# Kernel tuning notes

Hardware: AMD Instinct MI355X
Metric: run time of the kernel (lower is better)

The kernel has to match this reference:

```python
import jax, jax.numpy as jnp
import numpy as np

N_NODES = 50000
N_EDGES = 800000
N_GRAPHS = 256
F_IN = 256
H_DIM = 64


def setup_inputs() -> dict:
    key = jax.random.key(0)
    ks = jax.random.split(key, 9)
    x = jax.random.normal(ks[0], (N_NODES, F_IN), dtype=jnp.float32)
    edge_index = jax.random.randint(ks[1], (2, N_EDGES), 0, N_NODES, dtype=jnp.int64)
    batch = jnp.sort(jax.random.randint(ks[2], (N_NODES,), 0, N_GRAPHS, dtype=jnp.int64))
    s = 1.0 / np.sqrt(F_IN)
    Wq = jax.random.normal(ks[3], (F_IN, H_DIM), dtype=jnp.float32) * s
    bq = jnp.zeros((H_DIM,), dtype=jnp.float32)
    Wk = jax.random.normal(ks[4], (F_IN, H_DIM), dtype=jnp.float32) * s
    bk = jnp.zeros((H_DIM,), dtype=jnp.float32)
    Wv = jax.random.normal(ks[5], (F_IN, H_DIM), dtype=jnp.float32) * s
    bv = jnp.zeros((H_DIM,), dtype=jnp.float32)
    return {"x": x, "Wq": Wq, "bq": bq, "Wk": Wk, "bk": bk, "Wv": Wv, "bv": bv,
            "edge_index": edge_index, "batch": batch}


def reference(x, Wq, bq, Wk, bk, Wv, bv, edge_index, batch):
    src, dest = edge_index[0], edge_index[1]
    # node projections then per-edge gathers
    q = (x @ Wq + bq)[dest]            # [E, h]
    k = (x @ Wk + bk)[src]             # [E, h]
    v = (x @ Wv + bv)[src]             # [E, h]
    # per-edge dot-product score (bmm of [E,1,h] x [E,h,1])
    prod = jnp.sum(k * q, axis=-1, keepdims=True) / np.sqrt(H_DIM)  # [E, 1]
    exp = jnp.exp(prod)
    seg = batch[src]                   # per-graph segment of source node
    denom = jax.ops.segment_sum(exp, seg, num_segments=N_GRAPHS)    # [G, 1]
    a = exp / (denom[seg] + 1e-6)      # [E, 1]
    out = jax.ops.segment_sum(v * a, dest, num_segments=N_NODES)    # [N, h]
    return out
```

## Files before the change

### kernel.cpp

```cpp
#include <hip/hip_runtime.h>

#define H    64
#define F    256
#define NSEG 256
#define SCB  2048
#define MB   64
#define KC   64
#define XPAD 72

typedef float          f32x4v __attribute__((ext_vector_type(4)));
typedef short          bf16x8 __attribute__((ext_vector_type(8)));
typedef unsigned short u16x4  __attribute__((ext_vector_type(4)));

__global__ __launch_bounds__(256) void hist_kernel(
    const int* __restrict__ ei, int* __restrict__ counts8, int N, int E)
{
    const int pbase = (blockIdx.x & 7) * N;
    const int e0 = blockIdx.x * 1024 + threadIdx.x * 4;
    if (e0 + 3 < E) {
        const int4 d4 = *(const int4*)(ei + E + e0);
        atomicAdd(&counts8[pbase + min(max(d4.x, 0), N - 1)], 1);
        atomicAdd(&counts8[pbase + min(max(d4.y, 0), N - 1)], 1);
        atomicAdd(&counts8[pbase + min(max(d4.z, 0), N - 1)], 1);
        atomicAdd(&counts8[pbase + min(max(d4.w, 0), N - 1)], 1);
    } else {
        for (int e = e0; e < E; ++e) {
            int dst = ei[E + e];
            atomicAdd(&counts8[pbase + min(max(dst, 0), N - 1)], 1);
        }
    }
}

#define CVT_WRITE(buf, rr, cc, val) do {                                      \
    const float ff_[4] = {(val).x, (val).y, (val).z, (val).w};                \
    u16x4 h_, l_;                                                             \
    _Pragma("unroll")                                                         \
    for (int u_ = 0; u_ < 4; ++u_) {                                          \
        unsigned ub_ = __float_as_uint(ff_[u_]);                              \
        h_[u_] = (unsigned short)(ub_ >> 16);                                 \
        float rf_ = ff_[u_] - __uint_as_float(ub_ & 0xFFFF0000u);             \
        l_[u_] = (unsigned short)(__float_as_uint(rf_) >> 16);                \
    }                                                                         \
    *(u16x4*)&xs_hi[buf][(rr) * XPAD + (cc) * 4] = h_;                        \
    *(u16x4*)&xs_lo[buf][(rr) * XPAD + (cc) * 4] = l_;                        \
} while (0)

__global__ __launch_bounds__(768, 3) void qkv_mfma(
    const float* __restrict__ x,
    const float* __restrict__ Wq, const float* __restrict__ Wk,
    const float* __restrict__ Wv,
    const float* __restrict__ bq, const float* __restrict__ bk,
    const float* __restrict__ bv,
    float* __restrict__ q, float* __restrict__ k, float* __restrict__ v,
    int N, int ntiles)
{
    __shared__ unsigned short xs_hi[2][MB * XPAD];
    __shared__ unsigned short xs_lo[2][MB * XPAD];

    const int t    = threadIdx.x;
    const int lane = t & 63;
    const int w    = t >> 6;
    const int mat  = w >> 2;
    const int ct   = w & 3;
    const int l15  = lane & 15;
    const int quad = lane >> 4;

    const float* Wm   = (mat == 0) ? Wq : (mat == 1) ? Wk : Wv;
    const float* bias = (mat == 0) ? bq : (mat == 1) ? bk : bv;
    float*       dst  = (mat == 0) ? q  : (mat == 1) ? k  : v;
    const int col = ct * 16 + l15;
    const float bb = bias[col];

    bf16x8 Bh[8], Bl[8];
    #pragma unroll
    for (int u = 0; u < 8; ++u) {
        #pragma unroll
        for (int j = 0; j < 8; ++j) {
            const float f = Wm[(size_t)(u * 32 + quad * 8 + j) * H + col];
            const unsigned ub = __float_as_uint(f);
            Bh[u][j] = (short)(ub >> 16);
            const float rf = f - __uint_as_float(ub & 0xFFFF0000u);
            Bl[u][j] = (short)(__float_as_uint(rf) >> 16);
        }
    }

    const int r0 = t >> 4;
    const int c0 = t & 15;
    const int r1 = (t + 768) >> 4;

    #pragma unroll 1
    for (int tile = blockIdx.x; tile < ntiles; tile += gridDim.x) {
        const int block0 = tile * MB;

        f32x4v acc[4];
        #pragma unroll
        for (int i = 0; i < 4; ++i) acc[i] = (f32x4v)0.f;

        float4 pv0, pv1;
        pv0 = *(const float4*)(x + (size_t)min(block0 + r0, N - 1) * F + c0 * 4);
        if (t < 256)
            pv1 = *(const float4*)(x + (size_t)min(block0 + r1, N - 1) * F + c0 * 4);
        CVT_WRITE(0, r0, c0, pv0);
        if (t < 256) CVT_WRITE(0, r1, c0, pv1);

        #pragma unroll
        for (int c = 0; c < 4; ++c) {
            __syncthreads();

            if (c < 3) {
                const int kb = (c + 1) * KC;
                pv0 = *(const float4*)(x + (size_t)min(block0 + r0, N - 1) * F + kb + c0 * 4);
                if (t < 256)
                    pv1 = *(const float4*)(x + (size_t)min(block0 + r1, N - 1) * F + kb + c0 * 4);
            }

            #pragma unroll
            for (int sk = 0; sk < 2; ++sk) {
                const int u = c * 2 + sk;
                #pragma unroll
                for (int mt = 0; mt < 4; ++mt) {
                    const int ao = (mt * 16 + l15) * XPAD + sk * 32 + quad * 8;
                    const bf16x8 ah = *(const bf16x8*)&xs_hi[c & 1][ao];
                    const bf16x8 al = *(const bf16x8*)&xs_lo[c & 1][ao];
                    f32x4v a = acc[mt];
                    a = __builtin_amdgcn_mfma_f32_16x16x32_bf16(ah, Bh[u], a, 0, 0, 0);
                    a = __builtin_amdgcn_mfma_f32_16x16x32_bf16(ah, Bl[u], a, 0, 0, 0);
                    a = __builtin_amdgcn_mfma_f32_16x16x32_bf16(al, Bh[u], a, 0, 0, 0);
                    acc[mt] = a;
                }
            }

            if (c < 3) {
                const int nb = (c & 1) ^ 1;
                CVT_WRITE(nb, r0, c0, pv0);
                if (t < 256) CVT_WRITE(nb, r1, c0, pv1);
            }
        }

        #pragma unroll
        for (int mt = 0; mt < 4; ++mt) {
            #pragma unroll
            for (int r = 0; r < 4; ++r) {
                const int node = block0 + mt * 16 + quad * 4 + r;
                if (node < N)
                    dst[(size_t)node * H + col] = acc[mt][r] + bb;
            }
        }
    }
}

__global__ __launch_bounds__(256) void scanA(
    const int* __restrict__ counts8, int* __restrict__ counts,
    int* __restrict__ offsets, int* __restrict__ bsum, int n)
{
    __shared__ int ps[256];
    const int t = threadIdx.x;
    const int i0 = blockIdx.x * SCB + t * 8;
    int loc[8];
    int s = 0;
    #pragma unroll
    for (int u = 0; u < 8; ++u) {
        int i = i0 + u;
        int c = 0;
        if (i < n) {
            #pragma unroll
            for (int p = 0; p < 8; ++p) c += counts8[p * n + i];
            counts[i] = c;
            c = (c + 3) & ~3;
        }
        loc[u] = s; s += c;
    }
    ps[t] = s;
    __syncthreads();
    for (int off = 1; off < 256; off <<= 1) {
        int a = (t >= off) ? ps[t - off] : 0;
        __syncthreads();
        ps[t] += a;
        __syncthreads();
    }
    const int base = ps[t] - s;
    #pragma unroll
    for (int u = 0; u < 8; ++u) {
        int i = i0 + u;
        if (i < n) offsets[i] = base + loc[u];
    }
    if (t == 255) bsum[blockIdx.x] = ps[255];
}

__global__ void scanB(int* __restrict__ bsum, int nb)
{
    const int t = threadIdx.x;
    int v = (t < nb) ? bsum[t] : 0;
    int inc = v;
    #pragma unroll
    for (int off = 1; off < 64; off <<= 1) {
        int u = __shfl_up(inc, off, 64);
        if (t >= off) inc += u;
    }
    if (t < nb) bsum[t] = inc - v;
}

__global__ __launch_bounds__(256) void scanC(
    const int* __restrict__ bsum, const int* __restrict__ counts8,
    int* __restrict__ offsets, int* __restrict__ cursor8, int n)
{
    const int i0 = blockIdx.x * SCB + threadIdx.x * 8;
    const int add = bsum[blockIdx.x];
    #pragma unroll
    for (int u = 0; u < 8; ++u) {
        int i = i0 + u;
        if (i < n) {
            int o = offsets[i] + add;
            offsets[i] = o;
            #pragma unroll
            for (int p = 0; p < 8; ++p) {
                cursor8[p * n + i] = o;
                o += counts8[p * n + i];
            }
        }
    }
}

__global__ __launch_bounds__(256) void reorder_kernel(
    const int* __restrict__ ei, const int* __restrict__ batch,
    int* __restrict__ cursor8, unsigned* __restrict__ epack, int E, int N)
{
    const int pbase = (blockIdx.x & 7) * N;
    int e = blockIdx.x * 1024 + threadIdx.x;
    #pragma unroll
    for (int u = 0; u < 4; ++u) {
        if (e < E) {
            int src = ei[e];
            int dst = ei[E + e];
            src = min(max(src, 0), N - 1);
            dst = min(max(dst, 0), N - 1);
            int seg = batch[src];
            seg = min(max(seg, 0), NSEG - 1);
            int pos = atomicAdd(&cursor8[pbase + dst], 1);
            epack[pos] = (unsigned)src | ((unsigned)seg << 16);
        }
        e += 256;
    }
}

__global__ __launch_bounds__(256) void score_kernel(
    const float* __restrict__ q, const float* __restrict__ k,
    const unsigned* __restrict__ epack,
    const int* __restrict__ offsets, const int* __restrict__ counts,
    float* __restrict__ exps, float* __restrict__ denom8, int N)
{
    __shared__ float sden[NSEG];
    const int t = threadIdx.x;
    sden[t] = 0.f;
    __syncthreads();

    const int lane16 = t & 15;
    const int grp    = (t >> 4) & 3;
    const int wave   = t >> 6;
    const int nwaves = gridDim.x * 4;

    const float4* q4 = (const float4*)q;
    const float4* k4 = (const float4*)k;

    for (int n = blockIdx.x * 4 + wave; n < N; n += nwaves) {
        const int off = offsets[n];
        const int cnt = counts[n];
        if (cnt == 0) continue;
        const float4 qv = q4[(size_t)n * 16 + lane16];
        for (int i = grp; i < cnt; i += 4) {
            const int pos = off + i;
            const unsigned p = epack[pos];
            const int src = p & 0xFFFF;
            const float4 kv = k4[(size_t)src * 16 + lane16];
            float d = kv.x * qv.x + kv.y * qv.y + kv.z * qv.z + kv.w * qv.w;
            d += __shfl_xor(d, 1, 64);
            d += __shfl_xor(d, 2, 64);
            d += __shfl_xor(d, 4, 64);
            d += __shfl_xor(d, 8, 64);
            if (lane16 == 0) {
                float ex = __expf(d * 0.125f);
                exps[pos] = ex;
                atomicAdd(&sden[(p >> 16) & 255], ex);
            }
        }
    }
    __syncthreads();
    float ds = sden[t];
    if (ds != 0.f) atomicAdd(&denom8[(blockIdx.x & 7) * NSEG + t], ds);
}

__global__ __launch_bounds__(256) void accum_kernel(
    const float* __restrict__ v, const float* __restrict__ exps,
    const unsigned* __restrict__ epack,
    const int* __restrict__ offsets, const int* __restrict__ counts,
    const float* __restrict__ denom8, float* __restrict__ out, int N)
{
    __shared__ float rden[NSEG];
    const int t = threadIdx.x;
    {
        float dsum = 0.f;
        #pragma unroll
        for (int p = 0; p < 8; ++p) dsum += denom8[p * NSEG + t];
        rden[t] = 1.0f / (dsum + 1e-6f);
    }
    __syncthreads();

    const int lane = t & 63;
    const int wave = t >> 6;
    const int n = blockIdx.x * 4 + wave;
    if (n >= N) return;

    const int off = offsets[n];
    const int cnt = counts[n];

    float acc = 0.f;
    int i = 0;
    for (; i + 8 <= cnt; i += 8) {
        const uint4  pa = *(const uint4*)(epack + off + i);
        const uint4  pb = *(const uint4*)(epack + off + i + 4);
        const float4 ea = *(const float4*)(exps + off + i);
        const float4 eb = *(const float4*)(exps + off + i + 4);
        const float v0 = v[(size_t)(pa.x & 0xFFFF) * H + lane];
        const float v1 = v[(size_t)(pa.y & 0xFFFF) * H + lane];
        const float v2 = v[(size_t)(pa.z & 0xFFFF) * H + lane];
        const float v3 = v[(size_t)(pa.w & 0xFFFF) * H + lane];
        const float v4_ = v[(size_t)(pb.x & 0xFFFF) * H + lane];
        const float v5 = v[(size_t)(pb.y & 0xFFFF) * H + lane];
        const float v6 = v[(size_t)(pb.z & 0xFFFF) * H + lane];
        const float v7 = v[(size_t)(pb.w & 0xFFFF) * H + lane];
        acc = fmaf(v0, ea.x * rden[(pa.x >> 16) & 255], acc);
        acc = fmaf(v1, ea.y * rden[(pa.y >> 16) & 255], acc);
        acc = fmaf(v2, ea.z * rden[(pa.z >> 16) & 255], acc);
        acc = fmaf(v3, ea.w * rden[(pa.w >> 16) & 255], acc);
        acc = fmaf(v4_, eb.x * rden[(pb.x >> 16) & 255], acc);
        acc = fmaf(v5, eb.y * rden[(pb.y >> 16) & 255], acc);
        acc = fmaf(v6, eb.z * rden[(pb.z >> 16) & 255], acc);
        acc = fmaf(v7, eb.w * rden[(pb.w >> 16) & 255], acc);
    }
    for (; i + 4 <= cnt; i += 4) {
        const uint4  pp = *(const uint4*)(epack + off + i);
        const float4 ee = *(const float4*)(exps + off + i);
        const float v0 = v[(size_t)(pp.x & 0xFFFF) * H + lane];
        const float v1 = v[(size_t)(pp.y & 0xFFFF) * H + lane];
        const float v2 = v[(size_t)(pp.z & 0xFFFF) * H + lane];
        const float v3 = v[(size_t)(pp.w & 0xFFFF) * H + lane];
        acc = fmaf(v0, ee.x * rden[(pp.x >> 16) & 255], acc);
        acc = fmaf(v1, ee.y * rden[(pp.y >> 16) & 255], acc);
        acc = fmaf(v2, ee.z * rden[(pp.z >> 16) & 255], acc);
        acc = fmaf(v3, ee.w * rden[(pp.w >> 16) & 255], acc);
    }
    for (; i < cnt; ++i) {
        const unsigned p = epack[off + i];
        acc = fmaf(v[(size_t)(p & 0xFFFF) * H + lane],
                   exps[off + i] * rden[(p >> 16) & 255], acc);
    }
    out[(size_t)n * H + lane] = acc;
}

extern "C" void kernel_launch(void* const* d_in, const int* in_sizes, int n_in,
                              void* d_out, int out_size, void* d_ws, size_t ws_size,
                              hipStream_t stream)
{
    const float* x   = (const float*)d_in[0];
    const float* Wq  = (const float*)d_in[1];
    const float* bq  = (const float*)d_in[2];
    const float* Wk  = (const float*)d_in[3];
    const float* bk  = (const float*)d_in[4];
    const float* Wv  = (const float*)d_in[5];
    const float* bv  = (const float*)d_in[6];
    const int* ei    = (const int*)d_in[7];
    const int* batch = (const int*)d_in[8];

    const int N = in_sizes[8];
    const int E = in_sizes[7] / 2;
    const int EP = E + 3 * N + 16;

    float*    q       = (float*)d_ws;
    float*    k       = q + (size_t)N * H;
    float*    v       = k + (size_t)N * H;
    float*    exps    = v + (size_t)N * H;
    unsigned* epack   = (unsigned*)(exps + EP);
    int*      counts  = (int*)(epack + EP);
    int*      offsets = counts + N;
    int*      bsum    = offsets + N;
    float*    denom8  = (float*)(bsum + 64);

    int* counts8 = (int*)epack;
    int* cursor8 = (int*)exps;

    hipMemsetAsync(counts8, 0, 8 * (size_t)N * sizeof(int), stream);
    hipMemsetAsync(denom8, 0, 8 * NSEG * sizeof(float), stream);

    const int NT = (N + MB - 1) / MB;
    const int EB = (E + 1023) / 1024;
    const int NBSC = (N + SCB - 1) / SCB;

    hist_kernel<<<EB, 256, 0, stream>>>(ei, counts8, N, E);

    qkv_mfma<<<256, 768, 0, stream>>>(
        x, Wq, Wk, Wv, bq, bk, bv, q, k, v, N, NT);

    scanA<<<NBSC, 256, 0, stream>>>(counts8, counts, offsets, bsum, N);
    scanB<<<1, 64, 0, stream>>>(bsum, NBSC);
    scanC<<<NBSC, 256, 0, stream>>>(bsum, counts8, offsets, cursor8, N);

    reorder_kernel<<<(E + 1023) / 1024, 256, 0, stream>>>(
        ei, batch, cursor8, epack, E, N);

    score_kernel<<<2048, 256, 0, stream>>>(
        q, k, epack, offsets, counts, exps, denom8, N);

    accum_kernel<<<(N + 3) / 4, 256, 0, stream>>>(
        v, exps, epack, offsets, counts, denom8, (float*)d_out, N);
}
```

Baseline: 298.9 us.

## Replace 8-way privatized histogram with destination-range partitioned single counters

The hist and reorder kernels no longer keep eight private copies of the per-node counters and cursors. Each edge chunk is now processed by eight blocks, and each block only handles destinations inside its own node span, so there is a single counts and cursor array. This shrinks the memset and the scan work (no 8-way reductions or cursor expansions) and keeps atomics within a narrower address range, which should help cache locality. In exchange, the destination indices are read eight times and there are eight times as many blocks.

```diff
diff --git a/kernel.cpp b/kernel.cpp
--- a/kernel.cpp
+++ b/kernel.cpp
@@ -13,20 +13,25 @@
 typedef unsigned short u16x4  __attribute__((ext_vector_type(4)));
 
 __global__ __launch_bounds__(256) void hist_kernel(
-    const int* __restrict__ ei, int* __restrict__ counts8, int N, int E)
-{
-    const int pbase = (blockIdx.x & 7) * N;
-    const int e0 = blockIdx.x * 1024 + threadIdx.x * 4;
+    const int* __restrict__ ei, int* __restrict__ counts,
+    int N, int E, int nspan)
+{
+    const int p  = blockIdx.x & 7;
+    const int ci = blockIdx.x >> 3;
+    const int lo = p * nspan;
+    const int hi = min(N, lo + nspan);
+    const int e0 = ci * 1024 + threadIdx.x * 4;
     if (e0 + 3 < E) {
         const int4 d4 = *(const int4*)(ei + E + e0);
-        atomicAdd(&counts8[pbase + min(max(d4.x, 0), N - 1)], 1);
-        atomicAdd(&counts8[pbase + min(max(d4.y, 0), N - 1)], 1);
-        atomicAdd(&counts8[pbase + min(max(d4.z, 0), N - 1)], 1);
-        atomicAdd(&counts8[pbase + min(max(d4.w, 0), N - 1)], 1);
+        int d;
+        d = min(max(d4.x, 0), N - 1); if (d >= lo && d < hi) atomicAdd(&counts[d], 1);
+        d = min(max(d4.y, 0), N - 1); if (d >= lo && d < hi) atomicAdd(&counts[d], 1);
+        d = min(max(d4.z, 0), N - 1); if (d >= lo && d < hi) atomicAdd(&counts[d], 1);
+        d = min(max(d4.w, 0), N - 1); if (d >= lo && d < hi) atomicAdd(&counts[d], 1);
     } else {
         for (int e = e0; e < E; ++e) {
-            int dst = ei[E + e];
-            atomicAdd(&counts8[pbase + min(max(dst, 0), N - 1)], 1);
+            int d = min(max(ei[E + e], 0), N - 1);
+            if (d >= lo && d < hi) atomicAdd(&counts[d], 1);
         }
     }
 }
@@ -150,8 +155,8 @@
 }
 
 __global__ __launch_bounds__(256) void scanA(
-    const int* __restrict__ counts8, int* __restrict__ counts,
-    int* __restrict__ offsets, int* __restrict__ bsum, int n)
+    const int* __restrict__ counts, int* __restrict__ offsets,
+    int* __restrict__ bsum, int n)
 {
     __shared__ int ps[256];
     const int t = threadIdx.x;
@@ -161,13 +166,7 @@
     #pragma unroll
     for (int u = 0; u < 8; ++u) {
         int i = i0 + u;
-        int c = 0;
-        if (i < n) {
-            #pragma unroll
-            for (int p = 0; p < 8; ++p) c += counts8[p * n + i];
-            counts[i] = c;
-            c = (c + 3) & ~3;
-        }
+        int c = (i < n) ? ((counts[i] + 3) & ~3) : 0;
         loc[u] = s; s += c;
     }
     ps[t] = s;
@@ -201,45 +200,50 @@
 }
 
 __global__ __launch_bounds__(256) void scanC(
-    const int* __restrict__ bsum, const int* __restrict__ counts8,
-    int* __restrict__ offsets, int* __restrict__ cursor8, int n)
+    const int* __restrict__ bsum, int* __restrict__ offsets,
+    int* __restrict__ cursor, int n)
 {
     const int i0 = blockIdx.x * SCB + threadIdx.x * 8;
     const int add = bsum[blockIdx.x];
     #pragma unroll
     for (int u = 0; u < 8; ++u) {
         int i = i0 + u;
-        if (i < n) {
-            int o = offsets[i] + add;
-            offsets[i] = o;
-            #pragma unroll
-            for (int p = 0; p < 8; ++p) {
-                cursor8[p * n + i] = o;
-                o += counts8[p * n + i];
-            }
-        }
+        if (i < n) { int o = offsets[i] + add; offsets[i] = o; cursor[i] = o; }
     }
 }
 
 __global__ __launch_bounds__(256) void reorder_kernel(
     const int* __restrict__ ei, const int* __restrict__ batch,
-    int* __restrict__ cursor8, unsigned* __restrict__ epack, int E, int N)
-{
-    const int pbase = (blockIdx.x & 7) * N;
-    int e = blockIdx.x * 1024 + threadIdx.x;
+    int* __restrict__ cursor, unsigned* __restrict__ epack,
+    int E, int N, int nspan)
+{
+    const int p  = blockIdx.x & 7;
+    const int ci = blockIdx.x >> 3;
+    const int lo = p * nspan;
+    const int hi = min(N, lo + nspan);
+    const int e0 = ci * 1024 + threadIdx.x * 4;
+
+    int d[4];
+    if (e0 + 3 < E) {
+        const int4 d4 = *(const int4*)(ei + E + e0);
+        d[0] = d4.x; d[1] = d4.y; d[2] = d4.z; d[3] = d4.w;
+    } else {
+        #pragma unroll
+        for (int u = 0; u < 4; ++u)
+            d[u] = (e0 + u < E) ? ei[E + e0 + u] : -1;
+    }
+
     #pragma unroll
     for (int u = 0; u < 4; ++u) {
-        if (e < E) {
-            int src = ei[e];
-            int dst = ei[E + e];
+        const int dst = min(max(d[u], 0), N - 1);
+        if (d[u] >= 0 && dst >= lo && dst < hi) {
+            int src = ei[e0 + u];
             src = min(max(src, 0), N - 1);
-            dst = min(max(dst, 0), N - 1);
             int seg = batch[src];
             seg = min(max(seg, 0), NSEG - 1);
-            int pos = atomicAdd(&cursor8[pbase + dst], 1);
+            const int pos = atomicAdd(&cursor[dst], 1);
             epack[pos] = (unsigned)src | ((unsigned)seg << 16);
         }
-        e += 256;
     }
 }
 
@@ -382,30 +386,29 @@
     unsigned* epack   = (unsigned*)(exps + EP);
     int*      counts  = (int*)(epack + EP);
     int*      offsets = counts + N;
-    int*      bsum    = offsets + N;
+    int*      cursor  = offsets + N;
+    int*      bsum    = cursor + N;
     float*    denom8  = (float*)(bsum + 64);
 
-    int* counts8 = (int*)epack;
-    int* cursor8 = (int*)exps;
-
-    hipMemsetAsync(counts8, 0, 8 * (size_t)N * sizeof(int), stream);
+    hipMemsetAsync(counts, 0, N * sizeof(int), stream);
     hipMemsetAsync(denom8, 0, 8 * NSEG * sizeof(float), stream);
 
-    const int NT = (N + MB - 1) / MB;
-    const int EB = (E + 1023) / 1024;
-    const int NBSC = (N + SCB - 1) / SCB;
-
-    hist_kernel<<<EB, 256, 0, stream>>>(ei, counts8, N, E);
+    const int NT    = (N + MB - 1) / MB;
+    const int NC    = (E + 1023) / 1024;
+    const int nspan = (N + 7) / 8;
+    const int NBSC  = (N + SCB - 1) / SCB;
+
+    hist_kernel<<<8 * NC, 256, 0, stream>>>(ei, counts, N, E, nspan);
 
     qkv_mfma<<<256, 768, 0, stream>>>(
         x, Wq, Wk, Wv, bq, bk, bv, q, k, v, N, NT);
 
-    scanA<<<NBSC, 256, 0, stream>>>(counts8, counts, offsets, bsum, N);
+    scanA<<<NBSC, 256, 0, stream>>>(counts, offsets, bsum, N);
     scanB<<<1, 64, 0, stream>>>(bsum, NBSC);
-    scanC<<<NBSC, 256, 0, stream>>>(bsum, counts8, offsets, cursor8, N);
-
-    reorder_kernel<<<(E + 1023) / 1024, 256, 0, stream>>>(
-        ei, batch, cursor8, epack, E, N);
+    scanC<<<NBSC, 256, 0, stream>>>(bsum, offsets, cursor, N);
+
+    reorder_kernel<<<8 * NC, 256, 0, stream>>>(
+        ei, batch, cursor, epack, E, N, nspan);
 
     score_kernel<<<2048, 256, 0, stream>>>(
         q, k, epack, offsets, counts, exps, denom8, N);
```

Result: faster. 285.4 us (-4.5%).
